# Performance work log

Hardware: AMD Instinct MI355X
Metric: run time of the kernel (lower is better)

The kernel has to match this reference:

```python
import jax, jax.numpy as jnp
import numpy as np

B, S, H, NH, HD = 4, 2048, 2048, 16, 128
SCALE = HD ** -0.5


def rotate_half(x):
    x1, x2 = jnp.split(x, 2, axis=-1)
    return jnp.concatenate([-x2, x1], axis=-1)


def setup_inputs() -> dict:
    key = jax.random.key(0)
    ks = jax.random.split(key, 8)
    x = jax.random.normal(ks[0], (B, S, H), dtype=jnp.float32)
    # RoPE tables for positions 0..S-1, standard theta=10000 construction
    inv_freq = 1.0 / (10000.0 ** (jnp.arange(0, HD, 2, dtype=jnp.float32) / HD))
    t = jnp.arange(S, dtype=jnp.float32)
    freqs = jnp.einsum('s,d->sd', t, inv_freq)          # [S, HD/2]
    emb = jnp.concatenate([freqs, freqs], axis=-1)      # [S, HD]
    cos, sin = jnp.cos(emb), jnp.sin(emb)
    # causal mask: True = masked (future positions)
    mask = jnp.triu(jnp.ones((S, S), dtype=bool), k=1)
    std = H ** -0.5
    Wq = jax.random.normal(ks[1], (H, H), dtype=jnp.float32) * std
    Wk = jax.random.normal(ks[2], (H, H), dtype=jnp.float32) * std
    Wv = jax.random.normal(ks[3], (H, H), dtype=jnp.float32) * std
    Wo = jax.random.normal(ks[4], (H, H), dtype=jnp.float32) * std
    return {"x": x, "cos": cos, "sin": sin, "mask": mask,
            "Wq": Wq, "Wk": Wk, "Wv": Wv, "Wo": Wo}


def reference(x, cos, sin, mask, Wq, Wk, Wv, Wo):
    # projections: nn.Linear(bias=False) => x @ W.T
    def proj(W):
        y = jnp.einsum('bsh,ih->bsi', x, W)             # [B,S,inner]
        return y.reshape(B, S, NH, HD).transpose(0, 2, 1, 3)  # [B,NH,S,HD]
    q, k, v = proj(Wq), proj(Wk), proj(Wv)
    # RoPE (rotate-half), cos/sin broadcast over batch & heads
    c = cos[None, None, :, :]
    s = sin[None, None, :, :]
    q = q * c + rotate_half(q) * s
    k = k * c + rotate_half(k) * s
    # attention
    attn = jnp.einsum('bhqd,bhkd->bhqk', q, k) * SCALE
    attn = jnp.where(mask[None, None, :, :], -jnp.inf, attn)
    attn = jax.nn.softmax(attn, axis=-1)
    out = jnp.einsum('bhqk,bhkd->bhqd', attn, v)
    out = out.transpose(0, 2, 1, 3).reshape(B, S, NH * HD)
    y = jnp.einsum('bsi,hi->bsh', out, Wo)
    return y, k, v
```

## Files before the change

### kernel.cpp

```cpp
#include <hip/hip_runtime.h>
#include <hip/hip_bf16.h>
#include <math.h>

typedef __bf16 bf16_t;
typedef __bf16 bf16x8 __attribute__((ext_vector_type(8)));
typedef __bf16 bf16x4v __attribute__((ext_vector_type(4)));
typedef float  f32x4  __attribute__((ext_vector_type(4)));
typedef float  f32x16 __attribute__((ext_vector_type(16)));
typedef unsigned int u32x4 __attribute__((ext_vector_type(4)));

constexpr int CB = 4, CS = 2048, CH = 2048, CNH = 16, CHD = 128;
constexpr int CM = CB * CS;
constexpr float CSCALE = 0.08838834764831845f;
constexpr float CL2E   = 1.4426950408889634f;
constexpr float CSC2   = CSCALE * CL2E;

__device__ __forceinline__ float fexp2(float x) {
  float r;
  asm("v_exp_f32 %0, %1" : "=v"(r) : "v"(x));
  return r;
}

__device__ __forceinline__ void g2l16(const void* g, void* l) {
  __builtin_amdgcn_global_load_lds(
      (const __attribute__((address_space(1))) void*)g,
      (__attribute__((address_space(3))) void*)l, 16, 0, 0);
}

__global__ __launch_bounds__(256) void cvt_all(const float* __restrict__ x,
                                               const float* __restrict__ Wq,
                                               const float* __restrict__ Wk,
                                               const float* __restrict__ Wv,
                                               const float* __restrict__ Wo,
                                               bf16_t* __restrict__ xb,
                                               bf16_t* __restrict__ wqb,
                                               bf16_t* __restrict__ wkb,
                                               bf16_t* __restrict__ wvb,
                                               bf16_t* __restrict__ wob) {
  constexpr int NX = CM * CH / 4;
  constexpr int NW = CH * CH / 4;
  const int i = blockIdx.x * 256 + threadIdx.x;
  const float* src;
  bf16_t* dst;
  int off;
  if (i < NX) {
    src = x; dst = xb; off = i;
  } else {
    const int j = i - NX;
    const int sel = j / NW;
    off = j - sel * NW;
    src = (sel == 0) ? Wq : (sel == 1) ? Wk : (sel == 2) ? Wv : Wo;
    dst = (sel == 0) ? wqb : (sel == 1) ? wkb : (sel == 2) ? wvb : wob;
  }
  float4 v = reinterpret_cast<const float4*>(src)[off];
  bf16x4v o = {(bf16_t)v.x, (bf16_t)v.y, (bf16_t)v.z, (bf16_t)v.w};
  reinterpret_cast<bf16x4v*>(dst)[off] = o;
}

__device__ __forceinline__ void gemm256sq_core(const bf16_t* __restrict__ A,
                                               const bf16_t* __restrict__ Bm,
                                               bf16_t (*As2)[4][64 * 64],
                                               bf16_t (*Bs2)[4][64 * 64],
                                               int row0, int col0,
                                               f32x4 (&acc)[8][4]) {
  const int tid = threadIdx.x, lane = tid & 63, w = tid >> 6;
  const int wm = w >> 2, wn = w & 3;
  constexpr int NKT = CH / 64;
  const int id = w * 64 + lane;
  const int rl = id >> 3, ck = id & 7;

  auto stA = [&](int buf, int kt, int q) {
    const int row = q * 64 + rl;
    g2l16(A + (size_t)(row0 + row) * CH + kt * 64 + ((ck ^ (row & 7)) << 3),
          &As2[buf][q][id * 8]);
  };
  auto stB = [&](int buf, int kt, int q) {
    const int row = q * 64 + rl;
    g2l16(Bm + (size_t)(col0 + row) * CH + kt * 64 + ((ck ^ (row & 7)) << 3),
          &Bs2[buf][q][id * 8]);
  };
  auto rdA = [&](int buf, int r, int c) -> bf16x8 {
    return *(const bf16x8*)(&As2[buf][r >> 6][(r & 63) * 64 + ((c ^ (r & 7)) << 3)]);
  };
  auto rdB = [&](int buf, int r, int c) -> bf16x8 {
    return *(const bf16x8*)(&Bs2[buf][r >> 6][(r & 63) * 64 + ((c ^ (r & 7)) << 3)]);
  };

#pragma unroll
  for (int q = 0; q < 4; ++q) stB(0, 0, q);
#pragma unroll
  for (int q = 0; q < 4; ++q) stA(0, 0, q);
  asm volatile("s_waitcnt vmcnt(0)" ::: "memory");
  __builtin_amdgcn_s_barrier();
  __builtin_amdgcn_sched_barrier(0);

  const int ar0 = wm * 128 + (lane & 15);
  const int br0 = wn * 64 + (lane & 15);
  const int chi = lane >> 4;

  for (int t = 0; t < NKT; ++t) {
    const int buf = t & 1, nbuf = buf ^ 1;
    const bool pf = (t + 1 < NKT);
    bf16x8 bb[4][2], aa[2][2];

#pragma unroll
    for (int p = 0; p < 4; ++p) {
      if (p == 0) {
#pragma unroll
        for (int nf = 0; nf < 4; ++nf)
#pragma unroll
          for (int kk = 0; kk < 2; ++kk)
            bb[nf][kk] = rdB(buf, br0 + nf * 16, kk * 4 + chi);
      }
#pragma unroll
      for (int i = 0; i < 2; ++i)
#pragma unroll
        for (int kk = 0; kk < 2; ++kk)
          aa[i][kk] = rdA(buf, ar0 + (2 * p + i) * 16, kk * 4 + chi);

      if (pf) {
        if (p == 0) { stB(nbuf, t + 1, 0); stB(nbuf, t + 1, 1); }
        if (p == 1) { stA(nbuf, t + 1, 0); stA(nbuf, t + 1, 2); }
        if (p == 2) { stB(nbuf, t + 1, 2); stB(nbuf, t + 1, 3); }
        if (p == 3) { stA(nbuf, t + 1, 1); stA(nbuf, t + 1, 3); }
      }

      __builtin_amdgcn_s_barrier();
      asm volatile("s_waitcnt lgkmcnt(0)" ::: "memory");
      __builtin_amdgcn_sched_barrier(0);
      __builtin_amdgcn_s_setprio(1);
#pragma unroll
      for (int i = 0; i < 2; ++i)
#pragma unroll
        for (int nf = 0; nf < 4; ++nf)
#pragma unroll
          for (int kk = 0; kk < 2; ++kk)
            acc[2 * p + i][nf] = __builtin_amdgcn_mfma_f32_16x16x32_bf16(
                aa[i][kk], bb[nf][kk], acc[2 * p + i][nf], 0, 0, 0);
      __builtin_amdgcn_s_setprio(0);

      if (p == 1) {
        if (pf) { asm volatile("s_waitcnt vmcnt(4)" ::: "memory"); }
        else    { asm volatile("s_waitcnt vmcnt(0)" ::: "memory"); }
      }
      if (p == 3 && pf) { asm volatile("s_waitcnt vmcnt(2)" ::: "memory"); }
      __builtin_amdgcn_s_barrier();
      __builtin_amdgcn_sched_barrier(0);
    }
  }
}

__global__ __launch_bounds__(512, 1) void qkv_gemm(const bf16_t* __restrict__ xb,
                                                   const bf16_t* __restrict__ wqb,
                                                   const bf16_t* __restrict__ wkb,
                                                   const bf16_t* __restrict__ wvb,
                                                   bf16_t* __restrict__ qraw,
                                                   bf16_t* __restrict__ knat,
                                                   bf16_t* __restrict__ vt2,
                                                   float* __restrict__ vout) {
  __shared__ __align__(16) bf16_t LSD[2][2][4][64 * 64];
  const int z = blockIdx.z;
  const bf16_t* Bm = (z == 0) ? wqb : ((z == 1) ? wkb : wvb);
  const int row0 = blockIdx.x * 256, col0 = blockIdx.y * 256;
  f32x4 acc[8][4] = {};
  gemm256sq_core(xb, Bm, LSD[0], LSD[1], row0, col0, acc);

  const int tid = threadIdx.x, lane = tid & 63, w = tid >> 6;
  const int wm = w >> 2, wn = w & 3;

  bf16_t* L = &LSD[0][0][0][0];
#pragma unroll
  for (int i = 0; i < 8; ++i)
#pragma unroll
    for (int j = 0; j < 4; ++j) {
      const int col = wn * 64 + j * 16 + (lane & 15);
#pragma unroll
      for (int r = 0; r < 4; ++r) {
        const int row = wm * 128 + i * 16 + (lane >> 4) * 4 + r;
        L[row * 256 + (((col >> 3) ^ (row & 31)) << 3) + (col & 7)] =
            (bf16_t)acc[i][j][r];
      }
    }
  if (z == 2) {
#pragma unroll
    for (int i = 0; i < 8; ++i)
#pragma unroll
      for (int j = 0; j < 4; ++j) {
        const int gr0 = row0 + wm * 128 + i * 16 + (lane >> 4) * 4;
        const int gc = col0 + wn * 64 + j * 16 + (lane & 15);
        const int b = gr0 >> 11, s0 = gr0 & (CS - 1);
        const int nh = gc >> 7, hd = gc & (CHD - 1);
        const int bh = b * CNH + nh;
        bf16x4v pv = {(bf16_t)acc[i][j][0], (bf16_t)acc[i][j][1],
                      (bf16_t)acc[i][j][2], (bf16_t)acc[i][j][3]};
        *(bf16x4v*)(vt2 + (((size_t)bh * (CS / 16) + (s0 >> 4)) * CHD + hd) * 16 +
                    (s0 & 15)) = pv;
      }
  }
  __syncthreads();

  if (z == 0) {
#pragma unroll
    for (int k = 0; k < 16; ++k) {
      const int u = k * 512 + tid;
      const int row = u >> 5, ch = u & 31;
      bf16x8 v = *(const bf16x8*)&L[row * 256 + ((ch ^ (row & 31)) << 3)];
      const int gr = row0 + row, gc = col0 + ch * 8;
      const int b = gr >> 11, s = gr & (CS - 1), nh = gc >> 7, hd = gc & (CHD - 1);
      *(bf16x8*)&qraw[((size_t)(b * CNH + nh) * CS + s) * CHD + hd] = v;
    }
  } else if (z == 2) {
#pragma unroll
    for (int k = 0; k < 16; ++k) {
      const int u = k * 512 + tid;
      const int row = u >> 5, ch = u & 31;
      bf16x8 v = *(const bf16x8*)&L[row * 256 + ((ch ^ (row & 31)) << 3)];
      const int gr = row0 + row, gc = col0 + ch * 8;
      const int b = gr >> 11, s = gr & (CS - 1), nh = gc >> 7, hd = gc & (CHD - 1);
      float o[8];
#pragma unroll
      for (int e = 0; e < 8; ++e) o[e] = (float)v[e];
      float* vp = vout + ((size_t)(b * CNH + nh) * CS + s) * CHD + hd;
      *(float4*)(vp)     = *(float4*)(o);
      *(float4*)(vp + 4) = *(float4*)(o + 4);
    }
  } else {
#pragma unroll
    for (int k = 0; k < 16; ++k) {
      const int u = k * 512 + tid;
      const int s = u & 255, cc = u >> 8;
      bf16x8 v = *(const bf16x8*)&L[s * 256 + ((cc ^ (s & 31)) << 3)];
      const int gr = row0 + s, gc = col0 + cc * 8;
      const int b = gr >> 11, sg = gr & (CS - 1), nh = gc >> 7, hd = gc & (CHD - 1);
      const int pan = hd >> 4, half = (hd >> 3) & 1;
      *(bf16x8*)&knat[(((size_t)(b * CNH + nh) * 8 + pan) * CS + sg) * 16 +
                      half * 8] = v;
    }
  }
}

__global__ __launch_bounds__(512, 1) void y_gemm(const bf16_t* __restrict__ ob,
                                                 const bf16_t* __restrict__ wob,
                                                 float* __restrict__ yout) {
  __shared__ __align__(16) bf16_t LSD[2][2][4][64 * 64];
  const int row0 = blockIdx.x * 256, col0 = blockIdx.y * 256;
  f32x4 acc[8][4] = {};
  gemm256sq_core(ob, wob, LSD[0], LSD[1], row0, col0, acc);
  const int tid = threadIdx.x, lane = tid & 63, w = tid >> 6;
  const int wm = w >> 2, wn = w & 3;
  float* Lf = (float*)&LSD[0][0][0][0];

#pragma unroll
  for (int half = 0; half < 2; ++half) {
    if (wm == half) {
#pragma unroll
      for (int i = 0; i < 8; ++i)
#pragma unroll
        for (int j = 0; j < 4; ++j) {
          const int col = wn * 64 + j * 16 + (lane & 15);
#pragma unroll
          for (int r = 0; r < 4; ++r) {
            const int rl = i * 16 + (lane >> 4) * 4 + r;
            Lf[rl * 256 + col] = acc[i][j][r];
          }
        }
    }
    __syncthreads();
#pragma unroll
    for (int k = 0; k < 16; ++k) {
      const int u = k * 512 + tid;
      const int rl = u >> 6, ch = u & 63;
      float4 v = *(const float4*)&Lf[rl * 256 + ch * 4];
      const int gr = row0 + half * 128 + rl, gc = col0 + ch * 4;
      *(float4*)&yout[(size_t)gr * CH + gc] = v;
    }
    __syncthreads();
  }
}

__global__ __launch_bounds__(256) void rope_k(bf16_t* __restrict__ knat,
                                              const float* __restrict__ cosd,
                                              const float* __restrict__ sind,
                                              float* __restrict__ kout) {
  const int gid = blockIdx.x * 256 + threadIdx.x;
  const int row = gid >> 3, sub = gid & 7;
  const int pan = sub >> 1, hf = (sub & 1) * 8;
  const int bh = row >> 11, s = row & (CS - 1);
  const int d0 = pan * 16 + hf;
  bf16_t* k1 = knat + (((size_t)bh * 8 + pan) * CS + s) * 16 + hf;
  bf16_t* k2 = knat + (((size_t)bh * 8 + pan + 4) * CS + s) * 16 + hf;
  bf16x8 v1 = *(bf16x8*)k1;
  bf16x8 v2 = *(bf16x8*)k2;
  float c[8], sn[8];
  *(float4*)(c)      = *(const float4*)(cosd + s * CHD + d0);
  *(float4*)(c + 4)  = *(const float4*)(cosd + s * CHD + d0 + 4);
  *(float4*)(sn)     = *(const float4*)(sind + s * CHD + d0);
  *(float4*)(sn + 4) = *(const float4*)(sind + s * CHD + d0 + 4);
  float f1[8], f2[8];
  bf16x8 o1, o2;
#pragma unroll
  for (int i = 0; i < 8; ++i) {
    const float x1 = (float)v1[i], x2 = (float)v2[i];
    f1[i] = x1 * c[i] - x2 * sn[i];
    f2[i] = x2 * c[i] + x1 * sn[i];
    o1[i] = (bf16_t)f1[i];
    o2[i] = (bf16_t)f2[i];
  }
  *(bf16x8*)k1 = o1;
  *(bf16x8*)k2 = o2;
  const size_t kb = (size_t)row * CHD + d0;
  *(float4*)(kout + kb)          = *(float4*)(f1);
  *(float4*)(kout + kb + 4)      = *(float4*)(f1 + 4);
  *(float4*)(kout + kb + 64)     = *(float4*)(f2);
  *(float4*)(kout + kb + 64 + 4) = *(float4*)(f2 + 4);
}

__global__ __launch_bounds__(128, 3) void attn_kernel(const bf16_t* __restrict__ qb,
                                                      const bf16_t* __restrict__ kn,
                                                      const bf16_t* __restrict__ v2,
                                                      const float* __restrict__ cosd,
                                                      const float* __restrict__ sind,
                                                      bf16_t* __restrict__ ob) {
  __shared__ float Os[32][129];
  __shared__ float Ms[32], Ls[32];
  const int tid = threadIdx.x, lane = tid & 63, wh = tid >> 6;
  const int hi = lane >> 5, l31 = lane & 31;

  const int swz = (blockIdx.x & 7) * 512 + (blockIdx.x >> 3);
  const int bh = swz >> 6;
  const int qt = 63 - (swz & 63);

  const int b = bh >> 4, nh = bh & (CNH - 1);
  const bf16_t* kbase = kn + (size_t)bh * 8 * CS * 16;
  const bf16_t* vbase = v2 + (size_t)bh * (CS / 16) * CHD * 16;
  const int qw0 = qt * 32;
  const int qrow = qw0 + l31;

  bf16x8 bq[8];
  {
    const bf16_t* qp = qb + ((size_t)bh * CS + qrow) * CHD + hi * 8;
    bf16x8 raw[8];
#pragma unroll
    for (int ks = 0; ks < 8; ++ks) raw[ks] = *(const bf16x8*)(qp + ks * 16);
#pragma unroll
    for (int p = 0; p < 4; ++p) {
      const int d0 = p * 16 + hi * 8;
      float cc[8], ss[8];
      *(float4*)(cc)     = *(const float4*)(cosd + (size_t)qrow * CHD + d0);
      *(float4*)(cc + 4) = *(const float4*)(cosd + (size_t)qrow * CHD + d0 + 4);
      *(float4*)(ss)     = *(const float4*)(sind + (size_t)qrow * CHD + d0);
      *(float4*)(ss + 4) = *(const float4*)(sind + (size_t)qrow * CHD + d0 + 4);
#pragma unroll
      for (int e = 0; e < 8; ++e) {
        const float x1 = (float)raw[p][e], x2 = (float)raw[p + 4][e];
        bq[p][e]     = (bf16_t)(x1 * cc[e] - x2 * ss[e]);
        bq[p + 4][e] = (bf16_t)(x2 * cc[e] + x1 * ss[e]);
      }
    }
  }

  float m_ = -INFINITY, l_ = 0.f;
  f32x16 o_[4] = {};

  const int nt = (qt >> 1) + 1;
  for (int kt = wh; kt < nt; kt += 2) {
    const int kvb = kt * 64;

    f32x16 st[2] = {};
#pragma unroll
    for (int kb2 = 0; kb2 < 2; ++kb2) {
      bf16x8 ak[8];
      const bf16_t* kr = kbase + (size_t)(kvb + kb2 * 32 + l31) * 16 + hi * 8;
#pragma unroll
      for (int ks = 0; ks < 8; ++ks)
        ak[ks] = *(const bf16x8*)(kr + (size_t)ks * CS * 16);
#pragma unroll
      for (int ks = 0; ks < 8; ++ks)
        st[kb2] = __builtin_amdgcn_mfma_f32_32x32x16_bf16(ak[ks], bq[ks],
                                                          st[kb2], 0, 0, 0);
    }

    const bool anymask = (kvb + 63) > qw0;
#pragma unroll
    for (int blk = 0; blk < 2; ++blk)
#pragma unroll
      for (int r = 0; r < 16; ++r) {
        float xv = st[blk][r] * CSC2;
        if (anymask) {
          const int kv = kvb + blk * 32 + 4 * hi + (r & 3) + 8 * (r >> 2);
          if (kv > qrow) xv = -INFINITY;
        }
        st[blk][r] = xv;
      }

    float tmax = st[0][0];
#pragma unroll
    for (int r = 1; r < 16; ++r) tmax = fmaxf(tmax, st[0][r]);
#pragma unroll
    for (int r = 0; r < 16; ++r) tmax = fmaxf(tmax, st[1][r]);
    tmax = fmaxf(tmax, __shfl_xor(tmax, 32, 64));

    if (__any(tmax - m_ > 8.0f)) {
      const float mn = fmaxf(m_, tmax);
      const float corr = fexp2(m_ - mn);
      m_ = mn;
      l_ *= corr;
#pragma unroll
      for (int hb = 0; hb < 4; ++hb) o_[hb] *= corr;
    }

    float psum = 0.f;
#pragma unroll
    for (int blk = 0; blk < 2; ++blk)
#pragma unroll
      for (int r = 0; r < 16; ++r) {
        const float pv = fexp2(st[blk][r] - m_);
        st[blk][r] = pv;
        psum += pv;
      }
    psum += __shfl_xor(psum, 32, 64);
    l_ += psum;

    bf16x8 av[2][4];
    {
      const bf16_t* vr = vbase + ((size_t)(kvb >> 4) * CHD + l31) * 16 + hi * 8;
#pragma unroll
      for (int ks = 0; ks < 4; ++ks)
        av[0][ks] = *(const bf16x8*)(vr + (size_t)ks * CHD * 16);
    }

    bf16x8 pb[4];
#pragma unroll
    for (int ks = 0; ks < 4; ++ks) {
      const int blk = ks >> 1, r0 = (ks & 1) * 8;
      unsigned pw0, pw1, pw2, pw3;
      asm("v_cvt_pk_bf16_f32 %0, %1, %2" : "=v"(pw0) : "v"(st[blk][r0 + 0]), "v"(st[blk][r0 + 1]));
      asm("v_cvt_pk_bf16_f32 %0, %1, %2" : "=v"(pw2) : "v"(st[blk][r0 + 4]), "v"(st[blk][r0 + 5]));
      asm("v_cvt_pk_bf16_f32 %0, %1, %2" : "=v"(pw1) : "v"(st[blk][r0 + 2]), "v"(st[blk][r0 + 3]));
      asm("v_cvt_pk_bf16_f32 %0, %1, %2" : "=v"(pw3) : "v"(st[blk][r0 + 6]), "v"(st[blk][r0 + 7]));
      asm("v_permlane32_swap_b32 %0, %1" : "+v"(pw0), "+v"(pw2));
      asm("v_permlane32_swap_b32 %0, %1" : "+v"(pw1), "+v"(pw3));
      u32x4 pk = {pw0, pw1, pw2, pw3};
      pb[ks] = *reinterpret_cast<bf16x8*>(&pk);
    }

#pragma unroll
    for (int hb = 0; hb < 4; ++hb) {
      if (hb < 3) {
        const bf16_t* vr =
            vbase + ((size_t)(kvb >> 4) * CHD + (hb + 1) * 32 + l31) * 16 + hi * 8;
#pragma unroll
        for (int ks = 0; ks < 4; ++ks)
          av[(hb + 1) & 1][ks] = *(const bf16x8*)(vr + (size_t)ks * CHD * 16);
      }
#pragma unroll
      for (int ks = 0; ks < 4; ++ks)
        o_[hb] = __builtin_amdgcn_mfma_f32_32x32x16_bf16(av[hb & 1][ks], pb[ks],
                                                         o_[hb], 0, 0, 0);
    }
  }

  if (wh == 1) {
#pragma unroll
    for (int hb = 0; hb < 4; ++hb)
#pragma unroll
      for (int r = 0; r < 16; ++r) {
        const int hd = 32 * hb + 4 * hi + (r & 3) + 8 * (r >> 2);
        Os[l31][hd] = o_[hb][r];
      }
    if (hi == 0) { Ms[l31] = m_; Ls[l31] = l_; }
  }
  __builtin_amdgcn_s_barrier();
  if (wh == 1) return;

  const float m1 = Ms[l31], l1 = Ls[l31];
  const float mn = fmaxf(m_, m1);
  const float c0 = fexp2(m_ - mn), c1 = fexp2(m1 - mn);
  const float linv = 1.0f / (l_ * c0 + l1 * c1);
  bf16_t* orow = ob + ((size_t)(b * CS + qrow)) * CH + nh * CHD;
#pragma unroll
  for (int hb = 0; hb < 4; ++hb)
#pragma unroll
    for (int g = 0; g < 4; ++g) {
      const int hd0 = 32 * hb + 4 * hi + 8 * g;
      bf16x4v pv = {
          (bf16_t)((o_[hb][4 * g + 0] * c0 + Os[l31][hd0 + 0] * c1) * linv),
          (bf16_t)((o_[hb][4 * g + 1] * c0 + Os[l31][hd0 + 1] * c1) * linv),
          (bf16_t)((o_[hb][4 * g + 2] * c0 + Os[l31][hd0 + 2] * c1) * linv),
          (bf16_t)((o_[hb][4 * g + 3] * c0 + Os[l31][hd0 + 3] * c1) * linv)};
      *(bf16x4v*)(orow + hd0) = pv;
    }
}

extern "C" void kernel_launch(void* const* d_in, const int* in_sizes, int n_in,
                              void* d_out, int out_size, void* d_ws, size_t ws_size,
                              hipStream_t stream) {
  const float* x    = (const float*)d_in[0];
  const float* cosd = (const float*)d_in[1];
  const float* sind = (const float*)d_in[2];
  const float* Wq = (const float*)d_in[4];
  const float* Wk = (const float*)d_in[5];
  const float* Wv = (const float*)d_in[6];
  const float* Wo = (const float*)d_in[7];

  float* yout = (float*)d_out;
  float* kout = yout + (size_t)CM * CH;
  float* vout = kout + (size_t)CM * CH;

  char* ws = (char*)d_ws;
  size_t off = 0;
  auto wsalloc = [&](size_t bytes) {
    void* p = ws + off;
    off += (bytes + 255) & ~(size_t)255;
    return p;
  };
  bf16_t* xb   = (bf16_t*)wsalloc((size_t)CM * CH * 2);
  bf16_t* wqb  = (bf16_t*)wsalloc((size_t)CH * CH * 2);
  bf16_t* wkb  = (bf16_t*)wsalloc((size_t)CH * CH * 2);
  bf16_t* wvb  = (bf16_t*)wsalloc((size_t)CH * CH * 2);
  bf16_t* wob  = (bf16_t*)wsalloc((size_t)CH * CH * 2);
  bf16_t* qraw = (bf16_t*)wsalloc((size_t)CM * CH * 2);
  bf16_t* knat = (bf16_t*)wsalloc((size_t)CM * CH * 2);
  bf16_t* vt2  = (bf16_t*)wsalloc((size_t)CM * CH * 2);
  bf16_t* ob   = (bf16_t*)wsalloc((size_t)CM * CH * 2);

  cvt_all<<<(CM * CH / 4 + 4 * CH * CH / 4) / 256, 256, 0, stream>>>(
      x, Wq, Wk, Wv, Wo, xb, wqb, wkb, wvb, wob);

  qkv_gemm<<<dim3(CM / 256, CH / 256, 3), 512, 0, stream>>>(xb, wqb, wkb, wvb,
                                                            qraw, knat, vt2, vout);
  rope_k<<<CB * CNH * CS * 8 / 256, 256, 0, stream>>>(knat, cosd, sind, kout);
  attn_kernel<<<CB * CNH * (CS / 32), 128, 0, stream>>>(qraw, knat, vt2, cosd,
                                                        sind, ob);
  y_gemm<<<dim3(CM / 256, CH / 256), 512, 0, stream>>>(ob, wob, yout);
}
```

Baseline: 504.6 us.

## Load QKV GEMM B operand directly from global into registers, halve LDS footprint

The QKV projection GEMM now streams only the A tile (activations) through LDS, and each wave reads its weight fragments straight from global memory (via L2) into registers once per k-tile. LDS use drops to one double-buffered A tile. Because of that, the epilogue is split into two 128-row halves so the staging buffer fits. This aims to cut LDS traffic and barrier pressure for the B operand. The cost is uncoalesced, latency-exposed global loads of weights into registers, and an extra pair of syncs in the epilogue.

```diff
diff --git a/kernel.cpp b/kernel.cpp
--- a/kernel.cpp
+++ b/kernel.cpp
@@ -57,6 +57,182 @@
   reinterpret_cast<bf16x4v*>(dst)[off] = o;
 }
 
+__device__ __forceinline__ void gemmL2B_core(const bf16_t* __restrict__ A,
+                                             const bf16_t* __restrict__ Bm,
+                                             bf16_t (*As2)[4][64 * 64],
+                                             int row0, int col0,
+                                             f32x4 (&acc)[8][4]) {
+  const int tid = threadIdx.x, lane = tid & 63, w = tid >> 6;
+  const int wm = w >> 2, wn = w & 3;
+  constexpr int NKT = CH / 64;
+  const int rl = tid >> 3, ck = tid & 7;
+
+  auto stA = [&](int buf, int kt, int q) {
+    const int row = q * 64 + rl;
+    g2l16(A + (size_t)(row0 + row) * CH + kt * 64 + ((ck ^ (row & 7)) << 3),
+          &As2[buf][q][tid * 8]);
+  };
+  auto rdA = [&](int buf, int r, int c) -> bf16x8 {
+    return *(const bf16x8*)(&As2[buf][r >> 6][(r & 63) * 64 + ((c ^ (r & 7)) << 3)]);
+  };
+
+#pragma unroll
+  for (int q = 0; q < 4; ++q) stA(0, 0, q);
+  asm volatile("s_waitcnt vmcnt(0)" ::: "memory");
+  __builtin_amdgcn_s_barrier();
+  __builtin_amdgcn_sched_barrier(0);
+
+  const int ar0 = wm * 128 + (lane & 15);
+  const int bn0 = col0 + wn * 64 + (lane & 15);
+  const int bk0 = (lane >> 4) * 8;
+  const int chi = lane >> 4;
+  const int qorder[4] = {0, 2, 1, 3};
+
+  for (int t = 0; t < NKT; ++t) {
+    const int buf = t & 1, nbuf = buf ^ 1;
+    const bool pf = (t + 1 < NKT);
+
+    bf16x8 bb[4][2];
+#pragma unroll
+    for (int nf = 0; nf < 4; ++nf)
+#pragma unroll
+      for (int kk = 0; kk < 2; ++kk)
+        bb[nf][kk] = *(const bf16x8*)(Bm + (size_t)(bn0 + nf * 16) * CH +
+                                      t * 64 + kk * 32 + bk0);
+
+#pragma unroll
+    for (int p = 0; p < 4; ++p) {
+      if (pf) stA(nbuf, t + 1, qorder[p]);
+
+      bf16x8 aa[2][2];
+#pragma unroll
+      for (int i = 0; i < 2; ++i)
+#pragma unroll
+        for (int kk = 0; kk < 2; ++kk)
+          aa[i][kk] = rdA(buf, ar0 + (2 * p + i) * 16, kk * 4 + chi);
+
+      __builtin_amdgcn_s_setprio(1);
+#pragma unroll
+      for (int i = 0; i < 2; ++i)
+#pragma unroll
+        for (int nf = 0; nf < 4; ++nf)
+#pragma unroll
+          for (int kk = 0; kk < 2; ++kk)
+            acc[2 * p + i][nf] = __builtin_amdgcn_mfma_f32_16x16x32_bf16(
+                aa[i][kk], bb[nf][kk], acc[2 * p + i][nf], 0, 0, 0);
+      __builtin_amdgcn_s_setprio(0);
+
+      if (p == 1) {
+        if (pf) { asm volatile("s_waitcnt vmcnt(2)" ::: "memory"); }
+        else    { asm volatile("s_waitcnt vmcnt(0)" ::: "memory"); }
+        __builtin_amdgcn_s_barrier();
+        __builtin_amdgcn_sched_barrier(0);
+      }
+      if (p == 3) {
+        if (pf) { asm volatile("s_waitcnt vmcnt(2)" ::: "memory"); }
+        __builtin_amdgcn_s_barrier();
+        __builtin_amdgcn_sched_barrier(0);
+      }
+    }
+  }
+}
+
+__global__ __launch_bounds__(512, 1) void qkv_gemm(const bf16_t* __restrict__ xb,
+                                                   const bf16_t* __restrict__ wqb,
+                                                   const bf16_t* __restrict__ wkb,
+                                                   const bf16_t* __restrict__ wvb,
+                                                   bf16_t* __restrict__ qraw,
+                                                   bf16_t* __restrict__ knat,
+                                                   bf16_t* __restrict__ vt2,
+                                                   float* __restrict__ vout) {
+  __shared__ __align__(16) bf16_t As2[2][4][64 * 64];
+  const int z = blockIdx.z;
+  const bf16_t* Bm = (z == 0) ? wqb : ((z == 1) ? wkb : wvb);
+  const int row0 = blockIdx.x * 256, col0 = blockIdx.y * 256;
+  f32x4 acc[8][4] = {};
+  gemmL2B_core(xb, Bm, As2, row0, col0, acc);
+
+  const int tid = threadIdx.x, lane = tid & 63, w = tid >> 6;
+  const int wm = w >> 2, wn = w & 3;
+  bf16_t* L = &As2[0][0][0];
+
+  if (z == 2) {
+#pragma unroll
+    for (int i = 0; i < 8; ++i)
+#pragma unroll
+      for (int j = 0; j < 4; ++j) {
+        const int gr0 = row0 + wm * 128 + i * 16 + (lane >> 4) * 4;
+        const int gc = col0 + wn * 64 + j * 16 + (lane & 15);
+        const int b = gr0 >> 11, s0 = gr0 & (CS - 1);
+        const int nh = gc >> 7, hd = gc & (CHD - 1);
+        const int bh = b * CNH + nh;
+        bf16x4v pv = {(bf16_t)acc[i][j][0], (bf16_t)acc[i][j][1],
+                      (bf16_t)acc[i][j][2], (bf16_t)acc[i][j][3]};
+        *(bf16x4v*)(vt2 + (((size_t)bh * (CS / 16) + (s0 >> 4)) * CHD + hd) * 16 +
+                    (s0 & 15)) = pv;
+      }
+  }
+
+#pragma unroll
+  for (int half = 0; half < 2; ++half) {
+    __syncthreads();
+    if (wm == half) {
+#pragma unroll
+      for (int i = 0; i < 8; ++i)
+#pragma unroll
+        for (int j = 0; j < 4; ++j) {
+          const int col = wn * 64 + j * 16 + (lane & 15);
+#pragma unroll
+          for (int r = 0; r < 4; ++r) {
+            const int rl = i * 16 + (lane >> 4) * 4 + r;
+            L[rl * 256 + (((col >> 3) ^ (rl & 31)) << 3) + (col & 7)] =
+                (bf16_t)acc[i][j][r];
+          }
+        }
+    }
+    __syncthreads();
+
+    if (z == 0) {
+#pragma unroll
+      for (int k = 0; k < 8; ++k) {
+        const int u = k * 512 + tid;
+        const int rl = u >> 5, ch = u & 31;
+        bf16x8 v = *(const bf16x8*)&L[rl * 256 + ((ch ^ (rl & 31)) << 3)];
+        const int gr = row0 + half * 128 + rl, gc = col0 + ch * 8;
+        const int b = gr >> 11, s = gr & (CS - 1), nh = gc >> 7, hd = gc & (CHD - 1);
+        *(bf16x8*)&qraw[((size_t)(b * CNH + nh) * CS + s) * CHD + hd] = v;
+      }
+    } else if (z == 2) {
+#pragma unroll
+      for (int k = 0; k < 8; ++k) {
+        const int u = k * 512 + tid;
+        const int rl = u >> 5, ch = u & 31;
+        bf16x8 v = *(const bf16x8*)&L[rl * 256 + ((ch ^ (rl & 31)) << 3)];
+        const int gr = row0 + half * 128 + rl, gc = col0 + ch * 8;
+        const int b = gr >> 11, s = gr & (CS - 1), nh = gc >> 7, hd = gc & (CHD - 1);
+        float o[8];
+#pragma unroll
+        for (int e = 0; e < 8; ++e) o[e] = (float)v[e];
+        float* vp = vout + ((size_t)(b * CNH + nh) * CS + s) * CHD + hd;
+        *(float4*)(vp)     = *(float4*)(o);
+        *(float4*)(vp + 4) = *(float4*)(o + 4);
+      }
+    } else {
+#pragma unroll
+      for (int k = 0; k < 8; ++k) {
+        const int u = k * 512 + tid;
+        const int sl = u & 127, cc = u >> 7;
+        bf16x8 v = *(const bf16x8*)&L[sl * 256 + ((cc ^ (sl & 31)) << 3)];
+        const int gr = row0 + half * 128 + sl, gc = col0 + cc * 8;
+        const int b = gr >> 11, sg = gr & (CS - 1), nh = gc >> 7, hd = gc & (CHD - 1);
+        const int pan = hd >> 4, hf = (hd >> 3) & 1;
+        *(bf16x8*)&knat[(((size_t)(b * CNH + nh) * 8 + pan) * CS + sg) * 16 +
+                        hf * 8] = v;
+      }
+    }
+  }
+}
+
 __device__ __forceinline__ void gemm256sq_core(const bf16_t* __restrict__ A,
                                                const bf16_t* __restrict__ Bm,
                                                bf16_t (*As2)[4][64 * 64],
@@ -146,95 +322,6 @@
       if (p == 3 && pf) { asm volatile("s_waitcnt vmcnt(2)" ::: "memory"); }
       __builtin_amdgcn_s_barrier();
       __builtin_amdgcn_sched_barrier(0);
-    }
-  }
-}
-
-__global__ __launch_bounds__(512, 1) void qkv_gemm(const bf16_t* __restrict__ xb,
-                                                   const bf16_t* __restrict__ wqb,
-                                                   const bf16_t* __restrict__ wkb,
-                                                   const bf16_t* __restrict__ wvb,
-                                                   bf16_t* __restrict__ qraw,
-                                                   bf16_t* __restrict__ knat,
-                                                   bf16_t* __restrict__ vt2,
-                                                   float* __restrict__ vout) {
-  __shared__ __align__(16) bf16_t LSD[2][2][4][64 * 64];
-  const int z = blockIdx.z;
-  const bf16_t* Bm = (z == 0) ? wqb : ((z == 1) ? wkb : wvb);
-  const int row0 = blockIdx.x * 256, col0 = blockIdx.y * 256;
-  f32x4 acc[8][4] = {};
-  gemm256sq_core(xb, Bm, LSD[0], LSD[1], row0, col0, acc);
-
-  const int tid = threadIdx.x, lane = tid & 63, w = tid >> 6;
-  const int wm = w >> 2, wn = w & 3;
-
-  bf16_t* L = &LSD[0][0][0][0];
-#pragma unroll
-  for (int i = 0; i < 8; ++i)
-#pragma unroll
-    for (int j = 0; j < 4; ++j) {
-      const int col = wn * 64 + j * 16 + (lane & 15);
-#pragma unroll
-      for (int r = 0; r < 4; ++r) {
-        const int row = wm * 128 + i * 16 + (lane >> 4) * 4 + r;
-        L[row * 256 + (((col >> 3) ^ (row & 31)) << 3) + (col & 7)] =
-            (bf16_t)acc[i][j][r];
-      }
-    }
-  if (z == 2) {
-#pragma unroll
-    for (int i = 0; i < 8; ++i)
-#pragma unroll
-      for (int j = 0; j < 4; ++j) {
-        const int gr0 = row0 + wm * 128 + i * 16 + (lane >> 4) * 4;
-        const int gc = col0 + wn * 64 + j * 16 + (lane & 15);
-        const int b = gr0 >> 11, s0 = gr0 & (CS - 1);
-        const int nh = gc >> 7, hd = gc & (CHD - 1);
-        const int bh = b * CNH + nh;
-        bf16x4v pv = {(bf16_t)acc[i][j][0], (bf16_t)acc[i][j][1],
-                      (bf16_t)acc[i][j][2], (bf16_t)acc[i][j][3]};
-        *(bf16x4v*)(vt2 + (((size_t)bh * (CS / 16) + (s0 >> 4)) * CHD + hd) * 16 +
-                    (s0 & 15)) = pv;
-      }
-  }
-  __syncthreads();
-
-  if (z == 0) {
-#pragma unroll
-    for (int k = 0; k < 16; ++k) {
-      const int u = k * 512 + tid;
-      const int row = u >> 5, ch = u & 31;
-      bf16x8 v = *(const bf16x8*)&L[row * 256 + ((ch ^ (row & 31)) << 3)];
-      const int gr = row0 + row, gc = col0 + ch * 8;
-      const int b = gr >> 11, s = gr & (CS - 1), nh = gc >> 7, hd = gc & (CHD - 1);
-      *(bf16x8*)&qraw[((size_t)(b * CNH + nh) * CS + s) * CHD + hd] = v;
-    }
-  } else if (z == 2) {
-#pragma unroll
-    for (int k = 0; k < 16; ++k) {
-      const int u = k * 512 + tid;
-      const int row = u >> 5, ch = u & 31;
-      bf16x8 v = *(const bf16x8*)&L[row * 256 + ((ch ^ (row & 31)) << 3)];
-      const int gr = row0 + row, gc = col0 + ch * 8;
-      const int b = gr >> 11, s = gr & (CS - 1), nh = gc >> 7, hd = gc & (CHD - 1);
-      float o[8];
-#pragma unroll
-      for (int e = 0; e < 8; ++e) o[e] = (float)v[e];
-      float* vp = vout + ((size_t)(b * CNH + nh) * CS + s) * CHD + hd;
-      *(float4*)(vp)     = *(float4*)(o);
-      *(float4*)(vp + 4) = *(float4*)(o + 4);
-    }
-  } else {
-#pragma unroll
-    for (int k = 0; k < 16; ++k) {
-      const int u = k * 512 + tid;
-      const int s = u & 255, cc = u >> 8;
-      bf16x8 v = *(const bf16x8*)&L[s * 256 + ((cc ^ (s & 31)) << 3)];
-      const int gr = row0 + s, gc = col0 + cc * 8;
-      const int b = gr >> 11, sg = gr & (CS - 1), nh = gc >> 7, hd = gc & (CHD - 1);
-      const int pan = hd >> 4, half = (hd >> 3) & 1;
-      *(bf16x8*)&knat[(((size_t)(b * CNH + nh) * 8 + pan) * CS + sg) * 16 +
-                      half * 8] = v;
     }
   }
 }
```

New measurement: 621.5 us. 1.23x slower.
